# Performance work log

Hardware: AMD Instinct MI355X
Metric: run time of the kernel (lower is better)

## Reference

```python
import jax, jax.numpy as jnp
import numpy as np

B, T, N, H, W, C = 2, 3, 6, 256, 704, 17  # raster_shape=(256,704), 17 nuScenes classes
P = 500_000  # total supervised pixels across all (batch, time, camera) buckets


def setup_inputs() -> dict:
    key = jax.random.key(0)
    k1, k2, k3, k4, k5 = jax.random.split(key, 5)
    values = jax.random.normal(k1, (B, T, N, H, W, C), jnp.float32)
    idx_b = jax.random.randint(k2, (P,), 0, B)
    idx_t = jax.random.randint(k3, (P,), 0, T)
    idx_n = jax.random.randint(k4, (P,), 0, N)
    indices = jnp.stack([idx_b, idx_t, idx_n], axis=1).astype(jnp.int32)  # [P,3]
    # coors are (row, col) pixel coordinates in [0,H) x [0,W)
    coors = jax.random.uniform(k5, (P, 2), jnp.float32) * jnp.array([H, W], jnp.float32)
    return {"values": values, "indices": indices, "coors": coors}


def reference(values, indices, coors):
    # Faithful, fused version of GaussianFlowOccRasterizer.sample_indices:
    # the padded bucketize -> grid_sample -> re-gather pipeline equals direct
    # per-point bilinear sampling of image flat_idx[p] at pixel (coors[p]-0.5)
    # (grid_sample align_corners=False, padding_mode='zeros'); padded rows are
    # discarded by the final gather so they never affect the result.
    Bv, Tv, Nv, Hv, Wv, Cv = values.shape
    imgs = values.reshape(Bv * Tv * Nv, Hv, Wv, Cv)
    flat = indices[:, 0] * (Tv * Nv) + indices[:, 1] * Nv + indices[:, 2]  # [P]

    # grid = (coors[..., [1,0]] / [W, H]) * 2 - 1; unnormalized (align_corners=False):
    # pix = ((grid + 1) * size - 1) / 2  ==  coor - 0.5
    ix = coors[:, 1] - 0.5
    iy = coors[:, 0] - 0.5
    x0 = jnp.floor(ix)
    y0 = jnp.floor(iy)
    wx = ix - x0  # [P]
    wy = iy - y0
    x0i = x0.astype(jnp.int32)
    y0i = y0.astype(jnp.int32)

    def corner(xc, yc):
        inb = (xc >= 0) & (xc < Wv) & (yc >= 0) & (yc < Hv)
        v = imgs[flat, jnp.clip(yc, 0, Hv - 1), jnp.clip(xc, 0, Wv - 1)]  # [P,C]
        return jnp.where(inb[:, None], v, jnp.zeros((), values.dtype))

    v00 = corner(x0i, y0i)
    v01 = corner(x0i + 1, y0i)
    v10 = corner(x0i, y0i + 1)
    v11 = corner(x0i + 1, y0i + 1)

    wx = wx[:, None]
    wy = wy[:, None]
    out = (v00 * (1 - wx) * (1 - wy) + v01 * wx * (1 - wy)
           + v10 * (1 - wx) * wy + v11 * wx * wy)  # [P,C]
    return out
```

## Files before the change

kernel.cpp:

```cpp
#include <hip/hip_runtime.h>

#define B_ 2
#define T_ 3
#define N_ 6
#define H_ 256
#define W_ 704
#define C_ 17
#define P_ 500000

__global__ __launch_bounds__(256) void bilerp_gather_kernel(
    const float* __restrict__ values,
    const int*   __restrict__ indices,
    const float* __restrict__ coors,
    float*       __restrict__ out)
{
    int gid = blockIdx.x * blockDim.x + threadIdx.x;
    int p = gid >> 5;
    int c = gid & 31;
    if (p >= P_ || c >= C_) return;

    int ib = indices[p * 3 + 0];
    int it = indices[p * 3 + 1];
    int in = indices[p * 3 + 2];
    int flat = (ib * T_ + it) * N_ + in;

    float iy = coors[p * 2 + 0] - 0.5f;
    float ix = coors[p * 2 + 1] - 0.5f;
    float x0f = floorf(ix);
    float y0f = floorf(iy);
    float wx = ix - x0f;
    float wy = iy - y0f;
    int x0 = (int)x0f;
    int y0 = (int)y0f;
    int x1 = x0 + 1;
    int y1 = y0 + 1;

    const float* __restrict__ img = values + (size_t)flat * (H_ * W_ * C_);

    bool xin0 = (x0 >= 0) & (x0 < W_);
    bool xin1 = (x1 >= 0) & (x1 < W_);
    bool yin0 = (y0 >= 0) & (y0 < H_);
    bool yin1 = (y1 >= 0) & (y1 < H_);

    float v00 = 0.f, v01 = 0.f, v10 = 0.f, v11 = 0.f;
    if (yin0) {
        const float* row = img + (size_t)y0 * (W_ * C_);
        if (xin0) v00 = row[x0 * C_ + c];
        if (xin1) v01 = row[x1 * C_ + c];
    }
    if (yin1) {
        const float* row = img + (size_t)y1 * (W_ * C_);
        if (xin0) v10 = row[x0 * C_ + c];
        if (xin1) v11 = row[x1 * C_ + c];
    }

    float w00 = (1.f - wx) * (1.f - wy);
    float w01 = wx * (1.f - wy);
    float w10 = (1.f - wx) * wy;
    float w11 = wx * wy;

    out[p * C_ + c] = v00 * w00 + v01 * w01 + v10 * w10 + v11 * w11;
}

extern "C" void kernel_launch(void* const* d_in, const int* in_sizes, int n_in,
                              void* d_out, int out_size, void* d_ws, size_t ws_size,
                              hipStream_t stream)
{
    const float* values  = (const float*)d_in[0];
    const int*   indices = (const int*)d_in[1];
    const float* coors   = (const float*)d_in[2];
    float* out = (float*)d_out;

    const int threads_per_point = 32;
    const long long total_threads = (long long)P_ * threads_per_point;
    const int block = 256;
    const int grid = (int)((total_threads + block - 1) / block);

    bilerp_gather_kernel<<<grid, block, 0, stream>>>(values, indices, coors, out);
}
```

Before: 62.05 us.

## Pack three points per 64-lane wavefront and use clamped branchless corner loads

Remaps threads so each 64-wide wavefront serves three points with 17 lanes each, instead of one point per 32-thread slot with 15 idle lanes. This cuts the idle share of lanes and the number of blocks launched. Corner loads now always read from clamped coordinates, and out-of-bounds corners are zeroed through their weights rather than through branches. Output goes through nontemporal stores. The cost is a lane division by 17 and one idle lane per wave, plus unconditional loads for border points.

```diff
diff --git a/kernel.cpp b/kernel.cpp
--- a/kernel.cpp
+++ b/kernel.cpp
@@ -14,52 +14,58 @@
     const float* __restrict__ coors,
     float*       __restrict__ out)
 {
-    int gid = blockIdx.x * blockDim.x + threadIdx.x;
-    int p = gid >> 5;
-    int c = gid & 31;
-    if (p >= P_ || c >= C_) return;
+    const int tid  = threadIdx.x;
+    const int wave = blockIdx.x * (blockDim.x >> 6) + (tid >> 6);
+    const int lane = tid & 63;
+    const int sub  = lane / 17;
+    const int c    = lane - sub * 17;
+    const int p    = wave * 3 + sub;
+    if (sub >= 3 || p >= P_) return;
 
-    int ib = indices[p * 3 + 0];
-    int it = indices[p * 3 + 1];
-    int in = indices[p * 3 + 2];
-    int flat = (ib * T_ + it) * N_ + in;
+    const int ib = indices[p * 3 + 0];
+    const int it = indices[p * 3 + 1];
+    const int in = indices[p * 3 + 2];
+    const int flat = (ib * T_ + it) * N_ + in;
 
-    float iy = coors[p * 2 + 0] - 0.5f;
-    float ix = coors[p * 2 + 1] - 0.5f;
-    float x0f = floorf(ix);
-    float y0f = floorf(iy);
-    float wx = ix - x0f;
-    float wy = iy - y0f;
-    int x0 = (int)x0f;
-    int y0 = (int)y0f;
-    int x1 = x0 + 1;
-    int y1 = y0 + 1;
+    const float iy = coors[p * 2 + 0] - 0.5f;
+    const float ix = coors[p * 2 + 1] - 0.5f;
+    const float x0f = floorf(ix);
+    const float y0f = floorf(iy);
+    const float wx = ix - x0f;
+    const float wy = iy - y0f;
+    const int x0 = (int)x0f;
+    const int y0 = (int)y0f;
+    const int x1 = x0 + 1;
+    const int y1 = y0 + 1;
+
+    const int x0c = min(max(x0, 0), W_ - 1);
+    const int x1c = min(max(x1, 0), W_ - 1);
+    const int y0c = min(max(y0, 0), H_ - 1);
+    const int y1c = min(max(y1, 0), H_ - 1);
 
     const float* __restrict__ img = values + (size_t)flat * (H_ * W_ * C_);
 
-    bool xin0 = (x0 >= 0) & (x0 < W_);
-    bool xin1 = (x1 >= 0) & (x1 < W_);
-    bool yin0 = (y0 >= 0) & (y0 < H_);
-    bool yin1 = (y1 >= 0) & (y1 < H_);
+    const float v00 = img[((size_t)y0c * W_ + x0c) * C_ + c];
+    const float v01 = img[((size_t)y0c * W_ + x1c) * C_ + c];
+    const float v10 = img[((size_t)y1c * W_ + x0c) * C_ + c];
+    const float v11 = img[((size_t)y1c * W_ + x1c) * C_ + c];
 
-    float v00 = 0.f, v01 = 0.f, v10 = 0.f, v11 = 0.f;
-    if (yin0) {
-        const float* row = img + (size_t)y0 * (W_ * C_);
-        if (xin0) v00 = row[x0 * C_ + c];
-        if (xin1) v01 = row[x1 * C_ + c];
-    }
-    if (yin1) {
-        const float* row = img + (size_t)y1 * (W_ * C_);
-        if (xin0) v10 = row[x0 * C_ + c];
-        if (xin1) v11 = row[x1 * C_ + c];
-    }
+    const bool xin0 = (x0 >= 0) & (x0 < W_);
+    const bool xin1 = (x1 >= 0) & (x1 < W_);
+    const bool yin0 = (y0 >= 0) & (y0 < H_);
+    const bool yin1 = (y1 >= 0) & (y1 < H_);
 
     float w00 = (1.f - wx) * (1.f - wy);
     float w01 = wx * (1.f - wy);
     float w10 = (1.f - wx) * wy;
     float w11 = wx * wy;
+    w00 = (xin0 & yin0) ? w00 : 0.f;
+    w01 = (xin1 & yin0) ? w01 : 0.f;
+    w10 = (xin0 & yin1) ? w10 : 0.f;
+    w11 = (xin1 & yin1) ? w11 : 0.f;
 
-    out[p * C_ + c] = v00 * w00 + v01 * w01 + v10 * w10 + v11 * w11;
+    const float r = v00 * w00 + v01 * w01 + v10 * w10 + v11 * w11;
+    __builtin_nontemporal_store(r, &out[(size_t)p * C_ + c]);
 }
 
 extern "C" void kernel_launch(void* const* d_in, const int* in_sizes, int n_in,
@@ -71,10 +77,9 @@
     const float* coors   = (const float*)d_in[2];
     float* out = (float*)d_out;
 
-    const int threads_per_point = 32;
-    const long long total_threads = (long long)P_ * threads_per_point;
     const int block = 256;
-    const int grid = (int)((total_threads + block - 1) / block);
+    const int points_per_block = 12;
+    const int grid = (P_ + points_per_block - 1) / points_per_block;
 
     bilerp_gather_kernel<<<grid, block, 0, stream>>>(values, indices, coors, out);
 }
```

New measurement: 50.71 us (median of 2 runs). 1.22x faster.
